# Optimization experiments

Measured on AMD Instinct MI355X. Metric: run time of the kernel, lower is better.

## Reference

```python
import jax, jax.numpy as jnp
import numpy as np

# Static graph dimensions (mirror mat_wann config)
B, IN_DIM, NH, NO = 16384, 512, 128, 256
DENSITY = 0.03


def _build_adjacency():
    """Build the static sparse connectivity matrix.

    mat is [NH + NO, IN_DIM + NH]; entry values: 0 = no edge, 1 = linear edge
    (weight only), 2/3/4 = weight then tanh/relu/sigmoid. Hidden rows only read
    input columns (hidden->hidden block zero), output rows read inputs+hiddens.
    Edge order (for weight assignment) is row-major, as in the torch module.
    """
    rng = np.random.default_rng(0)
    p = DENSITY
    probs = [1.0 - p, p / 4, p / 4, p / 4, p / 4]
    mat_h = rng.choice(5, size=(NH, IN_DIM), p=probs)            # hidden rows (input cols only)
    mat_o = rng.choice(5, size=(NO, IN_DIM + NH), p=probs)       # output rows
    rows_h, cols_h = np.nonzero(mat_h)
    acts_h = mat_h[rows_h, cols_h]
    rows_o, cols_o = np.nonzero(mat_o)
    acts_o = mat_o[rows_o, cols_o]
    return (rows_h.astype(np.int32), cols_h.astype(np.int32), acts_h.astype(np.int32),
            rows_o.astype(np.int32), cols_o.astype(np.int32), acts_o.astype(np.int32))


def setup_inputs() -> dict:
    rows_h, cols_h, acts_h, rows_o, cols_o, acts_o = _build_adjacency()
    key = jax.random.key(0)
    kx, kh, ko = jax.random.split(key, 3)
    x = jax.random.normal(kx, (B, IN_DIM), dtype=jnp.float32)
    # one learned scalar weight per edge (nn.Linear(1,1,bias=False) each)
    wh = jax.random.normal(kh, (rows_h.shape[0],), dtype=jnp.float32) * 0.5
    wo = jax.random.normal(ko, (rows_o.shape[0],), dtype=jnp.float32) * 0.5
    return {
        "x": x, "wh": wh, "wo": wo,
        "rows_h": jnp.asarray(rows_h), "cols_h": jnp.asarray(cols_h), "acts_h": jnp.asarray(acts_h),
        "rows_o": jnp.asarray(rows_o), "cols_o": jnp.asarray(cols_o), "acts_o": jnp.asarray(acts_o),
    }


def _edge_act(z, acts):
    # act id 1 -> identity (weight only); 2 -> tanh; 3 -> relu; 4 -> sigmoid
    return jnp.where(acts == 2, jnp.tanh(z),
           jnp.where(acts == 3, jax.nn.relu(z),
           jnp.where(acts == 4, jax.nn.sigmoid(z), z)))


def reference(x, wh, wo, rows_h, cols_h, acts_h, rows_o, cols_o, acts_o):
    # hidden nodes: per-edge scalar weight + per-edge activation, scatter-add to dest
    zh = _edge_act(x[:, cols_h] * wh, acts_h)                     # [B, Eh]
    H = jnp.zeros((x.shape[0], NH), x.dtype).at[:, rows_h].add(zh)  # [B, NH]
    src = jnp.concatenate([x, H], axis=1)                         # [B, IN+NH]
    zo = _edge_act(src[:, cols_o] * wo, acts_o)                   # [B, Eo]
    out = jnp.zeros((x.shape[0], NO), x.dtype).at[:, rows_o].add(zo)
    return jnp.tanh(out)                                          # output_activation
```

## Files before the change

kernel.cpp:

```cpp
#include <hip/hip_runtime.h>
#include <math.h>

#define BATCH   16384
#define IN_DIM  512
#define NH      128
#define NO      256
#define L2E     1.4426950408889634f

__device__ __forceinline__ float fast_rcp(float x) { return __builtin_amdgcn_rcpf(x); }
__device__ __forceinline__ float fast_exp2(float x) {
#if __has_builtin(__builtin_amdgcn_exp2f)
    return __builtin_amdgcn_exp2f(x);
#else
    return exp2f(x);
#endif
}
__device__ __forceinline__ int rfl(int v) { return __builtin_amdgcn_readfirstlane(v); }
__device__ __forceinline__ int rdl(int v, int l) { return __builtin_amdgcn_readlane(v, l); }

__device__ __forceinline__ float fast_tanh(float z) {
    float ex = fast_exp2(2.f * L2E * z);
    return 1.f - 2.f * fast_rcp(1.f + ex);
}
__device__ __forceinline__ float act_k(int a) {
    return (a == 2) ? (2.f * L2E) : ((a == 4) ? -L2E : 0.f);
}

__device__ __forceinline__ unsigned int f2bf_rne(float f) {
    unsigned int u = __float_as_uint(f);
    return (u + 0x7FFFu + ((u >> 16) & 1u)) >> 16;
}
__device__ __forceinline__ float bf2f(unsigned short h) { return __uint_as_float(((unsigned int)h) << 16); }
__device__ __forceinline__ unsigned short f2bf16s(float f) { return (unsigned short)f2bf_rne(f); }

__device__ __forceinline__ int lower_bound_dev(const int* __restrict__ arr, int n, int v) {
    int lo = 0, hi = n;
    while (lo < hi) { int m = (lo + hi) >> 1; if (arr[m] < v) lo = m + 1; else hi = m; }
    return lo;
}

#define FXS     514
#define FHS     65
#define MLDS    99072
#define RSTRIDE 128

__global__ __launch_bounds__(512)
void prep_rows(const int* __restrict__ rows_h, const int* __restrict__ cols_h,
               const int* __restrict__ acts_h, const float* __restrict__ wh,
               const int* __restrict__ rows_o, const int* __restrict__ cols_o,
               const int* __restrict__ acts_o, const float* __restrict__ wo,
               int Eh, int Eo, uint2* __restrict__ rrh, uint2* __restrict__ rro)
{
    const int lane = (int)(threadIdx.x & 63);
    const int wid  = (int)((blockIdx.x * 512 + threadIdx.x) >> 6);
    if (wid >= NH + NO) return;
    const bool isH = wid < NH;
    const int r = isH ? wid : wid - NH;
    const int*   rows = isH ? rows_h : rows_o;
    const int*   cols = isH ? cols_h : cols_o;
    const int*   acts = isH ? acts_h : acts_o;
    const float* ww   = isH ? wh : wo;
    const int    E    = isH ? Eh : Eo;
    uint2* rec = (isH ? rrh : rro) + (size_t)r * RSTRIDE;

    const int e0 = lower_bound_dev(rows, E, r);
    const int e1 = lower_bound_dev(rows, E, r + 1);
    int n = e1 - e0; if (n > 127) n = 127;
    const unsigned long long lt = (1ull << lane) - 1ull;

    int cnt[8] = {0,0,0,0,0,0,0,0};
    for (int g = 0; g < n; g += 64) {
        int seg = -1;
        if (g + lane < n) {
            int e = e0 + g + lane;
            int a = acts[e];
            int col = cols[e];
            seg = (a - 1) + ((!isH && col >= IN_DIM) ? 4 : 0);
        }
        #pragma unroll
        for (int s = 0; s < 8; ++s) cnt[s] += __popcll(__ballot(seg == s));
    }
    int cum[9]; cum[0] = 0;
    #pragma unroll
    for (int s = 0; s < 8; ++s) cum[s + 1] = cum[s] + cnt[s];
    if (lane == 0) {
        unsigned hx = (unsigned)cum[1] | ((unsigned)cum[2] << 8) | ((unsigned)cum[3] << 16) | ((unsigned)cum[4] << 24);
        unsigned hy = (unsigned)cum[5] | ((unsigned)cum[6] << 8) | ((unsigned)cum[7] << 16) | ((unsigned)n << 24);
        rec[0] = make_uint2(hx, hy);
    }
    int pos[8];
    #pragma unroll
    for (int s = 0; s < 8; ++s) pos[s] = cum[s];
    for (int g = 0; g < n; g += 64) {
        int seg = -1; unsigned offv = 0, wbits = 0;
        if (g + lane < n) {
            int e = e0 + g + lane;
            int a = acts[e];
            int col = cols[e];
            bool hs = (!isH && col >= IN_DIM);
            seg = (a - 1) + (hs ? 4 : 0);
            offv = hs ? (unsigned)((col - IN_DIM) * FHS) : (unsigned)col;
            float w = ww[e];
            float ws = (a == 2) ? (2.f * L2E) * w : ((a == 4) ? -L2E * w : w);
            wbits = __float_as_uint(ws);
        }
        #pragma unroll
        for (int s = 0; s < 8; ++s) {
            unsigned long long m = __ballot(seg == s);
            if (seg == s) {
                int slot = 1 + pos[s] + __popcll(m & lt);
                rec[slot] = make_uint2(offv, wbits);
            }
            pos[s] += __popcll(m);
        }
    }
}

template<int ACT>
__device__ __forceinline__ float edge_apply(float acc, float v, float w) {
    if (ACT == 1)      return fmaf(v, w, acc);
    else if (ACT == 2) { float ex = fast_exp2(v * w); return acc + (1.f - 2.f * fast_rcp(1.f + ex)); }
    else if (ACT == 3) return acc + fmaxf(v * w, 0.f);
    else               { float ex = fast_exp2(v * w); return acc + fast_rcp(1.f + ex); }
}

template<int ACT, bool HSRC>
__device__ __forceinline__ void seg_run(float& acc,
                                        const unsigned short* __restrict__ Xl,
                                        const float* __restrict__ Hl,
                                        uint2 hv, int lo, int hi)
{
    int j = lo;
    #pragma unroll 2
    for (; j + 3 < hi; j += 4) {
        int o0 = rdl((int)hv.x, j + 1);
        int o1 = rdl((int)hv.x, j + 2);
        int o2 = rdl((int)hv.x, j + 3);
        int o3 = rdl((int)hv.x, j + 4);
        float v0 = HSRC ? Hl[o0] : bf2f(Xl[o0]);
        float v1 = HSRC ? Hl[o1] : bf2f(Xl[o1]);
        float v2 = HSRC ? Hl[o2] : bf2f(Xl[o2]);
        float v3 = HSRC ? Hl[o3] : bf2f(Xl[o3]);
        float w0 = __uint_as_float((unsigned)rdl((int)hv.y, j + 1));
        float w1 = __uint_as_float((unsigned)rdl((int)hv.y, j + 2));
        float w2 = __uint_as_float((unsigned)rdl((int)hv.y, j + 3));
        float w3 = __uint_as_float((unsigned)rdl((int)hv.y, j + 4));
        acc = edge_apply<ACT>(acc, v0, w0);
        acc = edge_apply<ACT>(acc, v1, w1);
        acc = edge_apply<ACT>(acc, v2, w2);
        acc = edge_apply<ACT>(acc, v3, w3);
    }
    for (; j < hi; ++j) {
        int o = rdl((int)hv.x, j + 1);
        float v = HSRC ? Hl[o] : bf2f(Xl[o]);
        float w = __uint_as_float((unsigned)rdl((int)hv.y, j + 1));
        acc = edge_apply<ACT>(acc, v, w);
    }
}

template<bool OUT>
__device__ __forceinline__ float row_body(uint2 hv, const uint2* __restrict__ grow,
                                          const unsigned short* __restrict__ Xl,
                                          const float* __restrict__ Hl)
{
    const int ux = rdl((int)hv.x, 0), uy = rdl((int)hv.y, 0);
    const int c1 = ux & 255, c2 = (ux >> 8) & 255, c3 = (ux >> 16) & 255, c4 = (int)((unsigned)ux >> 24);
    const int c5 = uy & 255, c6 = (uy >> 8) & 255, c7 = (uy >> 16) & 255, n  = (int)((unsigned)uy >> 24);
    float acc = 0.f;
    if (n <= 63) {
        seg_run<1,false>(acc, Xl, Hl, hv, 0,  c1);
        seg_run<2,false>(acc, Xl, Hl, hv, c1, c2);
        seg_run<3,false>(acc, Xl, Hl, hv, c2, c3);
        seg_run<4,false>(acc, Xl, Hl, hv, c3, c4);
        if (OUT) {
            seg_run<1,true>(acc, Xl, Hl, hv, c4, c5);
            seg_run<2,true>(acc, Xl, Hl, hv, c5, c6);
            seg_run<3,true>(acc, Xl, Hl, hv, c6, c7);
            seg_run<4,true>(acc, Xl, Hl, hv, c7, n);
        }
    } else {
        for (int j = 0; j < n; ++j) {
            int soff = rfl((int)grow[1 + j].x);
            float w  = __int_as_float(rfl((int)grow[1 + j].y));
            int seg = (j < c1) ? 0 : (j < c2) ? 1 : (j < c3) ? 2 : (j < c4) ? 3
                    : (j < c5) ? 4 : (j < c6) ? 5 : (j < c7) ? 6 : 7;
            float v = (seg >= 4) ? Hl[soff] : bf2f(Xl[soff]);
            int a = (seg & 3) + 1;
            if (a == 1) acc = fmaf(v, w, acc);
            else if (a == 2) { float ex = fast_exp2(v * w); acc += 1.f - 2.f * fast_rcp(1.f + ex); }
            else if (a == 3) acc += fmaxf(v * w, 0.f);
            else { float ex = fast_exp2(v * w); acc += fast_rcp(1.f + ex); }
        }
    }
    return acc;
}

__global__ __launch_bounds__(1024)
void fused_main(const float* __restrict__ x,
                const uint2* __restrict__ rrh, const uint2* __restrict__ rro,
                float* __restrict__ out)
{
    extern __shared__ char lds[];
    unsigned short* X   = (unsigned short*)lds;
    float*          Hf  = (float*)(lds + 65792);
    float*          OBT = (float*)lds;
    const int tid  = (int)threadIdx.x;
    const int lane = tid & 63;
    const int wv   = tid >> 6;
    const int rb   = (int)blockIdx.x * 64;
    const unsigned short* Xl = X + (size_t)lane * FXS;
    const float*          Hl = Hf + lane;

    {
        const float4* xv = (const float4*)(x + (size_t)rb * IN_DIM);
        #pragma unroll
        for (int kk = 0; kk < 8; ++kk) {
            int v = tid + kk * 1024;
            int rr = v >> 7, i = v & 127;
            float4 f = xv[v];
            unsigned int lo = f2bf_rne(f.x) | (f2bf_rne(f.y) << 16);
            unsigned int hi = f2bf_rne(f.z) | (f2bf_rne(f.w) << 16);
            unsigned int* dst = (unsigned int*)&X[rr * FXS + i * 4];
            dst[0] = lo; dst[1] = hi;
        }
    }
    __syncthreads();

    {
        uint2 hv = rrh[(size_t)(wv * 8) * RSTRIDE + lane];
        for (int q = 0; q < 8; ++q) {
            const int r = wv * 8 + q;
            uint2 hvn = hv;
            if (q < 7) hvn = rrh[(size_t)(r + 1) * RSTRIDE + lane];
            float acc = row_body<false>(hv, rrh + (size_t)r * RSTRIDE, Xl, Hl);
            Hf[r * FHS + lane] = acc;
            hv = hvn;
        }
    }
    __syncthreads();

    float res[NO / 16];
    {
        uint2 hv = rro[(size_t)(wv * 16) * RSTRIDE + lane];
        #pragma unroll 1
        for (int q = 0; q < 16; ++q) {
            const int r = wv * 16 + q;
            uint2 hvn = hv;
            if (q < 15) hvn = rro[(size_t)(r + 1) * RSTRIDE + lane];
            res[q] = fast_tanh(row_body<true>(hv, rro + (size_t)r * RSTRIDE, Xl, Hl));
            hv = hvn;
        }
    }
    __syncthreads();

    #pragma unroll
    for (int q = 0; q < NO / 16; ++q)
        OBT[(wv * (NO / 16) + q) * FHS + lane] = res[q];
    __syncthreads();
    #pragma unroll
    for (int s = 0; s < 4; ++s) {
        const int b = wv * 4 + s;
        #pragma unroll
        for (int i = 0; i < 4; ++i) {
            const int c = lane + i * 64;
            out[(size_t)(rb + b) * NO + c] = OBT[c * FHS + b];
        }
    }
}

#define FT      1024
#define FBPB    64
#define FHS2    65
#define FOBTS   260
#define FLDS    (99072 + 1544)
__device__ __forceinline__ float edge_act2(float z, int a, float k) {
    float ex = fast_exp2(k * z);
    float rc = fast_rcp(1.f + ex);
    return (a == 2) ? (1.f - 2.f * rc) : ((a == 4) ? rc : ((a == 3) ? fmaxf(z, 0.f) : z));
}
__global__ __launch_bounds__(FT)
void wann_fused(const float* __restrict__ x,
                const int* __restrict__ rows_h, const int* __restrict__ cols_h,
                const int* __restrict__ acts_h, const float* __restrict__ wh,
                const int* __restrict__ rows_o, const int* __restrict__ cols_o,
                const int* __restrict__ acts_o, const float* __restrict__ wo,
                float* __restrict__ out, int Eh, int Eo)
{
    extern __shared__ char lds[];
    unsigned short* X   = (unsigned short*)lds;
    float*          H   = (float*)(lds + 65792);
    float*          OBT = (float*)lds;
    int*            offsH = (int*)(lds + 99072);
    int*            offsO = offsH + (NH + 1);
    const int tid  = threadIdx.x;
    const int lane = tid & 63;
    const int wv   = tid >> 6;
    const int rb   = blockIdx.x * FBPB;
    const int* wh_i = (const int*)wh;
    const int* wo_i = (const int*)wo;
    {
        const float4* xv = (const float4*)(x + (size_t)rb * IN_DIM);
        #pragma unroll
        for (int kk = 0; kk < (FBPB * IN_DIM / 4) / FT; ++kk) {
            int v = tid + kk * FT;
            int r = v >> 7, i = v & 127;
            float4 f = xv[v];
            unsigned int lo = (unsigned int)f2bf16s(f.x) | ((unsigned int)f2bf16s(f.y) << 16);
            unsigned int hi = (unsigned int)f2bf16s(f.z) | ((unsigned int)f2bf16s(f.w) << 16);
            unsigned int* dst = (unsigned int*)&X[r * FXS + i * 4];
            dst[0] = lo; dst[1] = hi;
        }
    }
    if (tid <= NH) offsH[tid] = lower_bound_dev(rows_h, Eh, tid);
    else if (tid <= NH + 1 + NO) offsO[tid - (NH + 1)] = lower_bound_dev(rows_o, Eo, tid - (NH + 1));
    __syncthreads();
    for (int r = wv * (NH / 16); r < (wv + 1) * (NH / 16); ++r) {
        const int e0 = rfl(offsH[r]); const int e1 = rfl(offsH[r + 1]);
        float acc = 0.f;
        #pragma unroll 4
        for (int e = e0; e < e1; ++e) {
            int col = rfl(cols_h[e]); int a = rfl(acts_h[e]);
            float w = __int_as_float(rfl(wh_i[e]));
            acc += edge_act2(bf2f(X[lane * FXS + col]) * w, a, act_k(a));
        }
        H[r * FHS2 + lane] = acc;
    }
    __syncthreads();
    float res[NO / 16];
    #pragma unroll
    for (int rr = 0; rr < NO / 16; ++rr) {
        const int r = wv * (NO / 16) + rr;
        const int e0 = rfl(offsO[r]); const int e1 = rfl(offsO[r + 1]);
        float acc = 0.f;
        #pragma unroll 4
        for (int e = e0; e < e1; ++e) {
            int col = rfl(cols_o[e]); int a = rfl(acts_o[e]);
            float w = __int_as_float(rfl(wo_i[e]));
            float v = (col < IN_DIM) ? bf2f(X[lane * FXS + col]) : H[(col - IN_DIM) * FHS2 + lane];
            acc += edge_act2(v * w, a, act_k(a));
        }
        res[rr] = fast_tanh(acc);
    }
    __syncthreads();
    #pragma unroll
    for (int rr = 0; rr < NO / 16; ++rr)
        OBT[lane * FOBTS + wv * (NO / 16) + rr] = res[rr];
    __syncthreads();
    #pragma unroll
    for (int kk = 0; kk < (FBPB * NO / 4) / FT; ++kk) {
        int v = tid + kk * FT;
        int c4 = v & 63, b = v >> 6;
        float4 o = *(const float4*)&OBT[b * FOBTS + c4 * 4];
        *(float4*)&out[(size_t)(rb + b) * NO + c4 * 4] = o;
    }
}

extern "C" void kernel_launch(void* const* d_in, const int* in_sizes, int n_in,
                              void* d_out, int out_size, void* d_ws, size_t ws_size,
                              hipStream_t stream) {
    const float* x      = (const float*)d_in[0];
    const float* wh     = (const float*)d_in[1];
    const float* wo     = (const float*)d_in[2];
    const int*   rows_h = (const int*)d_in[3];
    const int*   cols_h = (const int*)d_in[4];
    const int*   acts_h = (const int*)d_in[5];
    const int*   rows_o = (const int*)d_in[6];
    const int*   cols_o = (const int*)d_in[7];
    const int*   acts_o = (const int*)d_in[8];
    float*       out    = (float*)d_out;

    const int Eh = in_sizes[1];
    const int Eo = in_sizes[2];

    char*  ws  = (char*)d_ws;
    uint2* rrh = (uint2*)ws;
    uint2* rro = (uint2*)(ws + (size_t)NH * RSTRIDE * 8);
    size_t need = (size_t)(NH + NO) * RSTRIDE * 8;

    if (ws_size >= need) {
        prep_rows<<<(NH + NO) * 64 / 512, 512, 0, stream>>>(
            rows_h, cols_h, acts_h, wh, rows_o, cols_o, acts_o, wo,
            Eh, Eo, rrh, rro);
        fused_main<<<BATCH / 64, 1024, MLDS, stream>>>(x, rrh, rro, out);
    } else {
        wann_fused<<<BATCH / FBPB, FT, FLDS, stream>>>(
            x, rows_h, cols_h, acts_h, wh, rows_o, cols_o, acts_o, wo, out, Eh, Eo);
    }
}
```

Measured before the change: 147.0 us.

## Pack edge offset and truncated weight into one 32-bit record word

Each edge record used to be a uint2 holding offset and weight. It is now a single 32-bit word: the offset sits in the low 10 bits and the weight, rounded to a reduced mantissa, in the high bits. Each row's records fit in one register per lane, so every edge needs one readlane instead of two, and the fast path covers up to 62 edges with a slower tail loop beyond that. The per-row sum is also split into two accumulators to break the dependency chain, and tanh's constant term is folded into the accumulator's initial value. The cost is lower weight precision, about 13 mantissa bits.

```diff
diff --git a/kernel.cpp b/kernel.cpp
--- a/kernel.cpp
+++ b/kernel.cpp
@@ -42,14 +42,15 @@
 #define FXS     514
 #define FHS     65
 #define MLDS    99072
-#define RSTRIDE 128
+#define RSU     128
+#define FASTN   62
 
 __global__ __launch_bounds__(512)
 void prep_rows(const int* __restrict__ rows_h, const int* __restrict__ cols_h,
                const int* __restrict__ acts_h, const float* __restrict__ wh,
                const int* __restrict__ rows_o, const int* __restrict__ cols_o,
                const int* __restrict__ acts_o, const float* __restrict__ wo,
-               int Eh, int Eo, uint2* __restrict__ rrh, uint2* __restrict__ rro)
+               int Eh, int Eo, unsigned* __restrict__ rrh, unsigned* __restrict__ rro)
 {
     const int lane = (int)(threadIdx.x & 63);
     const int wid  = (int)((blockIdx.x * 512 + threadIdx.x) >> 6);
@@ -61,11 +62,11 @@
     const int*   acts = isH ? acts_h : acts_o;
     const float* ww   = isH ? wh : wo;
     const int    E    = isH ? Eh : Eo;
-    uint2* rec = (isH ? rrh : rro) + (size_t)r * RSTRIDE;
+    unsigned* rec = (isH ? rrh : rro) + (size_t)r * RSU;
 
     const int e0 = lower_bound_dev(rows, E, r);
     const int e1 = lower_bound_dev(rows, E, r + 1);
-    int n = e1 - e0; if (n > 127) n = 127;
+    int n = e1 - e0; if (n > 126) n = 126;
     const unsigned long long lt = (1ull << lane) - 1ull;
 
     int cnt[8] = {0,0,0,0,0,0,0,0};
@@ -84,120 +85,118 @@
     #pragma unroll
     for (int s = 0; s < 8; ++s) cum[s + 1] = cum[s] + cnt[s];
     if (lane == 0) {
-        unsigned hx = (unsigned)cum[1] | ((unsigned)cum[2] << 8) | ((unsigned)cum[3] << 16) | ((unsigned)cum[4] << 24);
-        unsigned hy = (unsigned)cum[5] | ((unsigned)cum[6] << 8) | ((unsigned)cum[7] << 16) | ((unsigned)n << 24);
-        rec[0] = make_uint2(hx, hy);
+        rec[0] = (unsigned)cum[1] | ((unsigned)cum[2] << 8) | ((unsigned)cum[3] << 16) | ((unsigned)cum[4] << 24);
+        rec[1] = (unsigned)cum[5] | ((unsigned)cum[6] << 8) | ((unsigned)cum[7] << 16) | ((unsigned)n << 24);
     }
     int pos[8];
     #pragma unroll
     for (int s = 0; s < 8; ++s) pos[s] = cum[s];
     for (int g = 0; g < n; g += 64) {
-        int seg = -1; unsigned offv = 0, wbits = 0;
+        int seg = -1; unsigned payload = 0;
         if (g + lane < n) {
             int e = e0 + g + lane;
             int a = acts[e];
             int col = cols[e];
             bool hs = (!isH && col >= IN_DIM);
             seg = (a - 1) + (hs ? 4 : 0);
-            offv = hs ? (unsigned)((col - IN_DIM) * FHS) : (unsigned)col;
+            unsigned offv = hs ? (unsigned)(col - IN_DIM) : (unsigned)col;
             float w = ww[e];
             float ws = (a == 2) ? (2.f * L2E) * w : ((a == 4) ? -L2E * w : w);
-            wbits = __float_as_uint(ws);
+            unsigned wb = (__float_as_uint(ws) + 0x200u) & 0xFFFFFC00u;
+            payload = wb | offv;
         }
         #pragma unroll
         for (int s = 0; s < 8; ++s) {
             unsigned long long m = __ballot(seg == s);
-            if (seg == s) {
-                int slot = 1 + pos[s] + __popcll(m & lt);
-                rec[slot] = make_uint2(offv, wbits);
-            }
+            if (seg == s) rec[2 + pos[s] + __popcll(m & lt)] = payload;
             pos[s] += __popcll(m);
         }
     }
 }
 
 template<int ACT>
-__device__ __forceinline__ float edge_apply(float acc, float v, float w) {
+__device__ __forceinline__ float app(float acc, float v, float w) {
     if (ACT == 1)      return fmaf(v, w, acc);
-    else if (ACT == 2) { float ex = fast_exp2(v * w); return acc + (1.f - 2.f * fast_rcp(1.f + ex)); }
+    else if (ACT == 2) { float ex = fast_exp2(v * w); return fmaf(-2.f, fast_rcp(1.f + ex), acc); }
     else if (ACT == 3) return acc + fmaxf(v * w, 0.f);
     else               { float ex = fast_exp2(v * w); return acc + fast_rcp(1.f + ex); }
 }
 
-template<int ACT, bool HSRC>
-__device__ __forceinline__ void seg_run(float& acc,
+template<int ACT, bool HS>
+__device__ __forceinline__ void seg_run(float& a0, float& a1,
                                         const unsigned short* __restrict__ Xl,
                                         const float* __restrict__ Hl,
-                                        uint2 hv, int lo, int hi)
+                                        unsigned hv, int lo, int hi)
 {
     int j = lo;
     #pragma unroll 2
     for (; j + 3 < hi; j += 4) {
-        int o0 = rdl((int)hv.x, j + 1);
-        int o1 = rdl((int)hv.x, j + 2);
-        int o2 = rdl((int)hv.x, j + 3);
-        int o3 = rdl((int)hv.x, j + 4);
-        float v0 = HSRC ? Hl[o0] : bf2f(Xl[o0]);
-        float v1 = HSRC ? Hl[o1] : bf2f(Xl[o1]);
-        float v2 = HSRC ? Hl[o2] : bf2f(Xl[o2]);
-        float v3 = HSRC ? Hl[o3] : bf2f(Xl[o3]);
-        float w0 = __uint_as_float((unsigned)rdl((int)hv.y, j + 1));
-        float w1 = __uint_as_float((unsigned)rdl((int)hv.y, j + 2));
-        float w2 = __uint_as_float((unsigned)rdl((int)hv.y, j + 3));
-        float w3 = __uint_as_float((unsigned)rdl((int)hv.y, j + 4));
-        acc = edge_apply<ACT>(acc, v0, w0);
-        acc = edge_apply<ACT>(acc, v1, w1);
-        acc = edge_apply<ACT>(acc, v2, w2);
-        acc = edge_apply<ACT>(acc, v3, w3);
+        unsigned s0 = (unsigned)rdl((int)hv, j + 2);
+        unsigned s1 = (unsigned)rdl((int)hv, j + 3);
+        unsigned s2 = (unsigned)rdl((int)hv, j + 4);
+        unsigned s3 = (unsigned)rdl((int)hv, j + 5);
+        float v0 = HS ? Hl[(s0 & 1023u) * FHS] : bf2f(Xl[s0 & 1023u]);
+        float v1 = HS ? Hl[(s1 & 1023u) * FHS] : bf2f(Xl[s1 & 1023u]);
+        float v2 = HS ? Hl[(s2 & 1023u) * FHS] : bf2f(Xl[s2 & 1023u]);
+        float v3 = HS ? Hl[(s3 & 1023u) * FHS] : bf2f(Xl[s3 & 1023u]);
+        a0 = app<ACT>(a0, v0, __uint_as_float(s0 & 0xFFFFFC00u));
+        a1 = app<ACT>(a1, v1, __uint_as_float(s1 & 0xFFFFFC00u));
+        a0 = app<ACT>(a0, v2, __uint_as_float(s2 & 0xFFFFFC00u));
+        a1 = app<ACT>(a1, v3, __uint_as_float(s3 & 0xFFFFFC00u));
     }
     for (; j < hi; ++j) {
-        int o = rdl((int)hv.x, j + 1);
-        float v = HSRC ? Hl[o] : bf2f(Xl[o]);
-        float w = __uint_as_float((unsigned)rdl((int)hv.y, j + 1));
-        acc = edge_apply<ACT>(acc, v, w);
-    }
-}
+        unsigned sp = (unsigned)rdl((int)hv, j + 2);
+        float v = HS ? Hl[(sp & 1023u) * FHS] : bf2f(Xl[sp & 1023u]);
+        a0 = app<ACT>(a0, v, __uint_as_float(sp & 0xFFFFFC00u));
+    }
+}
+
+__device__ __forceinline__ int imin(int a, int b) { return a < b ? a : b; }
 
 template<bool OUT>
-__device__ __forceinline__ float row_body(uint2 hv, const uint2* __restrict__ grow,
+__device__ __forceinline__ float row_body(unsigned hv, const unsigned* __restrict__ grow,
                                           const unsigned short* __restrict__ Xl,
-                                          const float* __restrict__ Hl)
-{
-    const int ux = rdl((int)hv.x, 0), uy = rdl((int)hv.y, 0);
-    const int c1 = ux & 255, c2 = (ux >> 8) & 255, c3 = (ux >> 16) & 255, c4 = (int)((unsigned)ux >> 24);
-    const int c5 = uy & 255, c6 = (uy >> 8) & 255, c7 = (uy >> 16) & 255, n  = (int)((unsigned)uy >> 24);
-    float acc = 0.f;
-    if (n <= 63) {
-        seg_run<1,false>(acc, Xl, Hl, hv, 0,  c1);
-        seg_run<2,false>(acc, Xl, Hl, hv, c1, c2);
-        seg_run<3,false>(acc, Xl, Hl, hv, c2, c3);
-        seg_run<4,false>(acc, Xl, Hl, hv, c3, c4);
-        if (OUT) {
-            seg_run<1,true>(acc, Xl, Hl, hv, c4, c5);
-            seg_run<2,true>(acc, Xl, Hl, hv, c5, c6);
-            seg_run<3,true>(acc, Xl, Hl, hv, c6, c7);
-            seg_run<4,true>(acc, Xl, Hl, hv, c7, n);
-        }
-    } else {
-        for (int j = 0; j < n; ++j) {
-            int soff = rfl((int)grow[1 + j].x);
-            float w  = __int_as_float(rfl((int)grow[1 + j].y));
-            int seg = (j < c1) ? 0 : (j < c2) ? 1 : (j < c3) ? 2 : (j < c4) ? 3
-                    : (j < c5) ? 4 : (j < c6) ? 5 : (j < c7) ? 6 : 7;
-            float v = (seg >= 4) ? Hl[soff] : bf2f(Xl[soff]);
-            int a = (seg & 3) + 1;
-            if (a == 1) acc = fmaf(v, w, acc);
-            else if (a == 2) { float ex = fast_exp2(v * w); acc += 1.f - 2.f * fast_rcp(1.f + ex); }
-            else if (a == 3) acc += fmaxf(v * w, 0.f);
-            else { float ex = fast_exp2(v * w); acc += fast_rcp(1.f + ex); }
-        }
-    }
-    return acc;
+                                          const float* __restrict__ Hl, int lane)
+{
+    const unsigned hx = (unsigned)rdl((int)hv, 0);
+    const unsigned hy = (unsigned)rdl((int)hv, 1);
+    const int c1 = hx & 255, c2 = (hx >> 8) & 255, c3 = (hx >> 16) & 255, c4 = (int)(hx >> 24);
+    const int c5 = hy & 255, c6 = (hy >> 8) & 255, c7 = (hy >> 16) & 255, n  = (int)(hy >> 24);
+    const int m1 = imin(c1, FASTN), m2 = imin(c2, FASTN), m3 = imin(c3, FASTN), m4 = imin(c4, FASTN);
+    const int m5 = imin(c5, FASTN), m6 = imin(c6, FASTN), m7 = imin(c7, FASTN), m8 = imin(n, FASTN);
+    float a0 = (float)((m2 - m1) + (OUT ? (m6 - m5) : 0));
+    float a1 = 0.f;
+    seg_run<1,false>(a0, a1, Xl, Hl, hv, 0,  m1);
+    seg_run<2,false>(a0, a1, Xl, Hl, hv, m1, m2);
+    seg_run<3,false>(a0, a1, Xl, Hl, hv, m2, m3);
+    seg_run<4,false>(a0, a1, Xl, Hl, hv, m3, m4);
+    if (OUT) {
+        seg_run<1,true>(a0, a1, Xl, Hl, hv, m4, m5);
+        seg_run<2,true>(a0, a1, Xl, Hl, hv, m5, m6);
+        seg_run<3,true>(a0, a1, Xl, Hl, hv, m6, m7);
+        seg_run<4,true>(a0, a1, Xl, Hl, hv, m7, m8);
+    }
+    if (__builtin_expect(n > FASTN, 0)) {
+        unsigned hv2 = grow[64 + lane];
+        for (int j = FASTN; j < n; ++j) {
+            unsigned sp = (unsigned)rdl((int)hv2, j - FASTN);
+            int s = (j < c1) ? 0 : (j < c2) ? 1 : (j < c3) ? 2 : (j < c4) ? 3
+                  : (j < c5) ? 4 : (j < c6) ? 5 : (j < c7) ? 6 : 7;
+            float w = __uint_as_float(sp & 0xFFFFFC00u);
+            float v = (s >= 4) ? Hl[(sp & 1023u) * FHS] : bf2f(Xl[sp & 1023u]);
+            int a = (s & 3) + 1;
+            if (a == 1) a0 = fmaf(v, w, a0);
+            else if (a == 2) { float ex = fast_exp2(v * w); a0 += 1.f - 2.f * fast_rcp(1.f + ex); }
+            else if (a == 3) a0 += fmaxf(v * w, 0.f);
+            else { float ex = fast_exp2(v * w); a0 += fast_rcp(1.f + ex); }
+        }
+    }
+    return a0 + a1;
 }
 
 __global__ __launch_bounds__(1024)
 void fused_main(const float* __restrict__ x,
-                const uint2* __restrict__ rrh, const uint2* __restrict__ rro,
+                const unsigned* __restrict__ rrh, const unsigned* __restrict__ rro,
                 float* __restrict__ out)
 {
     extern __shared__ char lds[];
@@ -227,12 +226,12 @@
     __syncthreads();
 
     {
-        uint2 hv = rrh[(size_t)(wv * 8) * RSTRIDE + lane];
+        unsigned hv = rrh[(size_t)(wv * 8) * RSU + lane];
         for (int q = 0; q < 8; ++q) {
             const int r = wv * 8 + q;
-            uint2 hvn = hv;
-            if (q < 7) hvn = rrh[(size_t)(r + 1) * RSTRIDE + lane];
-            float acc = row_body<false>(hv, rrh + (size_t)r * RSTRIDE, Xl, Hl);
+            unsigned hvn = hv;
+            if (q < 7) hvn = rrh[(size_t)(r + 1) * RSU + lane];
+            float acc = row_body<false>(hv, rrh + (size_t)r * RSU, Xl, Hl, lane);
             Hf[r * FHS + lane] = acc;
             hv = hvn;
         }
@@ -241,13 +240,13 @@
 
     float res[NO / 16];
     {
-        uint2 hv = rro[(size_t)(wv * 16) * RSTRIDE + lane];
+        unsigned hv = rro[(size_t)(wv * 16) * RSU + lane];
         #pragma unroll 1
         for (int q = 0; q < 16; ++q) {
             const int r = wv * 16 + q;
-            uint2 hvn = hv;
-            if (q < 15) hvn = rro[(size_t)(r + 1) * RSTRIDE + lane];
-            res[q] = fast_tanh(row_body<true>(hv, rro + (size_t)r * RSTRIDE, Xl, Hl));
+            unsigned hvn = hv;
+            if (q < 15) hvn = rro[(size_t)(r + 1) * RSU + lane];
+            res[q] = fast_tanh(row_body<true>(hv, rro + (size_t)r * RSU, Xl, Hl, lane));
             hv = hvn;
         }
     }
@@ -372,10 +371,10 @@
     const int Eh = in_sizes[1];
     const int Eo = in_sizes[2];
 
-    char*  ws  = (char*)d_ws;
-    uint2* rrh = (uint2*)ws;
-    uint2* rro = (uint2*)(ws + (size_t)NH * RSTRIDE * 8);
-    size_t need = (size_t)(NH + NO) * RSTRIDE * 8;
+    char*     ws  = (char*)d_ws;
+    unsigned* rrh = (unsigned*)ws;
+    unsigned* rro = (unsigned*)(ws + (size_t)NH * RSU * 4);
+    size_t need = (size_t)(NH + NO) * RSU * 4;
 
     if (ws_size >= need) {
         prep_rows<<<(NH + NO) * 64 / 512, 512, 0, stream>>>(
```

Measured after the change: 144.6 us. About the same (-1.6%).
